# Performance work log

Measured on AMD Instinct MI355X. Metric: run time of the kernel, lower is better.

## Reference

```python
import jax, jax.numpy as jnp
import numpy as np

D_MODEL = 1024
N_HEADS = 16
D_HEAD = D_MODEL // N_HEADS


def setup_inputs() -> dict:
    key = jax.random.key(0)
    ks = jax.random.split(key, 9)
    s = 1.0 / np.sqrt(D_MODEL)
    def lin(kw, kb):
        W = jax.random.uniform(kw, (D_MODEL, D_MODEL), jnp.float32, -s, s)
        b = jax.random.uniform(kb, (D_MODEL,), jnp.float32, -s, s)
        return W, b
    Wq, bq = lin(ks[0], ks[1])
    Wk, bk = lin(ks[2], ks[3])
    Wv, bv = lin(ks[4], ks[5])
    Wo, bo = lin(ks[6], ks[7])
    x = jax.random.normal(ks[8], (4, 2048, D_MODEL), jnp.float32)
    return {"x": x, "Wq": Wq, "bq": bq, "Wk": Wk, "bk": bk,
            "Wv": Wv, "bv": bv, "Wo": Wo, "bo": bo}


def reference(x, Wq, bq, Wk, bk, Wv, bv, Wo, bo):
    B, T, C = x.shape
    # torch Linear: y = x @ W.T + b
    Q = x @ Wq.T + bq
    K = x @ Wk.T + bk
    V = x @ Wv.T + bv
    # [B, H, T, Dh]
    Q = Q.reshape(B, T, N_HEADS, D_HEAD).transpose(0, 2, 1, 3)
    K = K.reshape(B, T, N_HEADS, D_HEAD).transpose(0, 2, 1, 3)
    V = V.reshape(B, T, N_HEADS, D_HEAD).transpose(0, 2, 1, 3)
    scale = jnp.float32(np.sqrt(D_HEAD))
    scores = jnp.einsum('bhqd,bhkd->bhqk', Q, K) / scale
    causal = jnp.tril(jnp.ones((T, T), dtype=bool))  # True where allowed
    scores = jnp.where(causal, scores, jnp.float32(-jnp.inf))
    attn = jax.nn.softmax(scores, axis=-1)
    out = jnp.einsum('bhqk,bhkd->bhqd', attn, V)
    out = out.transpose(0, 2, 1, 3).reshape(B, T, C)
    return out @ Wo.T + bo
```

## Files before the change

kernel.cpp:

```cpp
#include <hip/hip_runtime.h>
#include <hip/hip_bf16.h>


typedef float f32x4 __attribute__((ext_vector_type(4)));
typedef __bf16 bf16x8 __attribute__((ext_vector_type(8)));

#define DEVI __device__ __forceinline__

#define QSCALE 0.1803368801111204f

template<int N> struct IC { static constexpr int value = N; };

DEVI ushort f2b(float x) {
  __hip_bfloat16 h = __float2bfloat16(x);
  return __builtin_bit_cast(ushort, h);
}

DEVI unsigned int pkbf(float a, float b) {
#if __has_builtin(__builtin_amdgcn_cvt_pk_bf16_f32)
  typedef __bf16 bf16x2 __attribute__((ext_vector_type(2)));
  bf16x2 r = __builtin_amdgcn_cvt_pk_bf16_f32(a, b);
  return __builtin_bit_cast(unsigned int, r);
#else
  return (unsigned int)f2b(a) | ((unsigned int)f2b(b) << 16);
#endif
}

DEVI bf16x8 ldsFrag(const ushort* p) {
  return __builtin_bit_cast(bf16x8, *(const uint4*)p);
}

DEVI f32x4 mfma16(bf16x8 a, bf16x8 b, f32x4 c) {
  return __builtin_amdgcn_mfma_f32_16x16x32_bf16(a, b, c, 0, 0, 0);
}

DEVI void gload_lds16(const ushort* g, ushort* l) {
  __builtin_amdgcn_global_load_lds(
      (const __attribute__((address_space(1))) unsigned int*)g,
      (__attribute__((address_space(3))) unsigned int*)l, 16, 0, 0);
}

__global__ void k_cvtAll(const float4* __restrict__ x,
                         const float4* __restrict__ w0, const float4* __restrict__ w1,
                         const float4* __restrict__ w2, const float4* __restrict__ w3,
                         ushort4* __restrict__ xb, ushort4* __restrict__ wcat) {
  const int blk = blockIdx.x;
  const int i = blk * 256 + threadIdx.x;
  float4 f;
  ushort4* dst;
  int di;
  if (blk < 8192) {
    f = x[i]; dst = xb; di = i;
  } else {
    const int wi = i - 8192 * 256;
    const int sel = wi >> 18;
    const float4* src = (sel == 0) ? w0 : (sel == 1) ? w1 : (sel == 2) ? w2 : w3;
    f = src[wi & 262143]; dst = wcat; di = wi;
  }
  ushort4 o;
  o.x = f2b(f.x); o.y = f2b(f.y); o.z = f2b(f.z); o.w = f2b(f.w);
  dst[di] = o;
}

template<int MODE>
__global__ __launch_bounds__(256)
void k_gemm(const ushort* __restrict__ A, const ushort* __restrict__ W,
            const float* __restrict__ b0, const float* __restrict__ b1,
            const float* __restrict__ b2, float* __restrict__ outF,
            ushort* __restrict__ oQ, ushort* __restrict__ oK, ushort* __restrict__ oV) {
  __shared__ ushort As[128 * 64];
  __shared__ ushort Bs[128 * 64];
  const int tid = threadIdx.x;
  const int wave = tid >> 6, lane = tid & 63;
  const int col = lane & 15, quad = lane >> 4;
  const int id = blockIdx.x;
  const int s_ = id >> 3;
  const int m0 = ((id & 7) * 8 + (s_ & 7)) * 128;
  const int n0 = (s_ >> 3) * 128;
  const int wm = (wave >> 1) * 64, wn = (wave & 1) * 64;
  f32x4 acc[4][4] = {};

  const int grow = lane >> 3;
  const int gchunk = ((lane & 7) ^ grow) * 8;
  const ushort* Ag = A + (size_t)(m0 + wave * 8 + grow) * 1024 + gchunk;
  const ushort* Wg = W + (size_t)(n0 + wave * 8 + grow) * 1024 + gchunk;
  ushort* AsW = &As[wave * 512];
  ushort* BsW = &Bs[wave * 512];

  const int matId = (MODE == 0) ? (n0 >> 10) : 0;
  const int cswz = col & 7;

  auto kloop = [&](auto swc) {
    constexpr bool SW = (decltype(swc)::value != 0);
    for (int k0 = 0; k0 < 1024; k0 += 64) {
      __syncthreads();
#pragma unroll
      for (int g = 0; g < 4; ++g) {
        gload_lds16(Ag + (size_t)g * 32 * 1024 + k0, AsW + g * 2048);
        gload_lds16(Wg + (size_t)g * 32 * 1024 + k0, BsW + g * 2048);
      }
      __syncthreads();
#pragma unroll
      for (int kk = 0; kk < 2; ++kk) {
        bf16x8 af[4], bfr[4];
#pragma unroll
        for (int i = 0; i < 4; ++i)
          af[i] = ldsFrag(&As[(wm + i * 16 + col) * 64 + (((kk * 4 + quad) ^ cswz) * 8)]);
#pragma unroll
        for (int j = 0; j < 4; ++j)
          bfr[j] = ldsFrag(&Bs[(wn + j * 16 + col) * 64 + (((kk * 4 + quad) ^ cswz) * 8)]);
#pragma unroll
        for (int i = 0; i < 4; ++i)
#pragma unroll
          for (int j = 0; j < 4; ++j) {
            if constexpr (SW)
              acc[i][j] = mfma16(bfr[j], af[i], acc[i][j]);
            else
              acc[i][j] = mfma16(af[i], bfr[j], acc[i][j]);
          }
      }
    }
  };

  if (MODE == 1 || matId < 2) kloop(IC<1>{}); else kloop(IC<0>{});

  if (MODE == 1) {
#pragma unroll
    for (int j = 0; j < 4; ++j) {
      const int nb = n0 + wn + j * 16 + quad * 4;
      const float4 bb = *(const float4*)&b0[nb];
#pragma unroll
      for (int i = 0; i < 4; ++i) {
        const int m = m0 + wm + i * 16 + col;
        float4 v;
        v.x = acc[i][j][0] + bb.x;
        v.y = acc[i][j][1] + bb.y;
        v.z = acc[i][j][2] + bb.z;
        v.w = acc[i][j][3] + bb.w;
        *(float4*)&outF[(size_t)m * 1024 + nb] = v;
      }
    }
  } else if (matId < 2) {
    ushort* dst = (matId == 0) ? oQ : oK;
    const float* bias = (matId == 0) ? b0 : b1;
    const float sc = (matId == 0) ? QSCALE : 1.0f;
#pragma unroll
    for (int j = 0; j < 4; ++j) {
      const int nl = ((n0 & 1023) + wn + j * 16 + quad * 4);
      const int h = nl >> 6, dh0 = nl & 63;
      const float4 bb = *(const float4*)&bias[nl];
#pragma unroll
      for (int i = 0; i < 4; ++i) {
        const int m = m0 + wm + i * 16 + col;
        const int b = m >> 11, t = m & 2047;
        ushort4 pk;
        pk.x = f2b((acc[i][j][0] + bb.x) * sc);
        pk.y = f2b((acc[i][j][1] + bb.y) * sc);
        pk.z = f2b((acc[i][j][2] + bb.z) * sc);
        pk.w = f2b((acc[i][j][3] + bb.w) * sc);
        *(ushort4*)&dst[(((size_t)(b * 16 + h) * 2048) + t) * 64 + dh0] = pk;
      }
    }
  } else {
#pragma unroll
    for (int j = 0; j < 4; ++j) {
      const int nl = ((n0 & 1023) + wn + j * 16 + col);
      const int h = nl >> 6, dh = nl & 63;
      const float bn = b2[nl];
#pragma unroll
      for (int i = 0; i < 4; ++i) {
        const int mBase = m0 + wm + i * 16 + quad * 4;
        const int b = mBase >> 11, t = mBase & 2047;
        ushort4 pk;
        pk.x = f2b(acc[i][j][0] + bn);
        pk.y = f2b(acc[i][j][1] + bn);
        pk.z = f2b(acc[i][j][2] + bn);
        pk.w = f2b(acc[i][j][3] + bn);
        *(ushort4*)&oV[(((size_t)(b * 16 + h) * 64) + dh) * 2048 + t] = pk;
      }
    }
  }
}

__global__ __launch_bounds__(512, 1)
void k_attn(const ushort* __restrict__ Q, const ushort* __restrict__ K,
            const ushort* __restrict__ Vt, ushort* __restrict__ AO) {
  __shared__ ushort Ks[2 * 4096];
  __shared__ ushort Vs[2 * 4096];
  __shared__ ushort Os[512];
  __shared__ ushort Ps[16 * 16 * 72];
  const int tid = threadIdx.x;
  const int wave = tid >> 6, lane = tid & 63;
  const int col = lane & 15, quad = lane >> 4;
  const int id = blockIdx.x;
  const int bh = (id & 7) * 8 + ((id >> 3) & 7);
  const int pr = id >> 6;
  const ushort* Qg = Q + (size_t)bh * 2048 * 64;
  const ushort* Kg = K + (size_t)bh * 2048 * 64;
  const ushort* Vg = Vt + (size_t)bh * 64 * 2048;

  if (tid < 128) {
    const ushort one = 0x3F80;
    ushort4 zv;
    if (tid < 8) { zv.x = one; zv.y = one; zv.z = one; zv.w = one; }
    else         { zv.x = 0;   zv.y = 0;   zv.z = 0;   zv.w = 0;   }
    *(ushort4*)&Os[tid * 4] = zv;
  }

  const int grow = lane >> 3;
  const int gchunk = ((lane & 7) ^ grow) * 8;
  const int cswz = col & 7;
  ushort* Pw0 = &Ps[((wave * 2 + 0) * 16 + col) * 72];
  ushort* Pw1 = &Ps[((wave * 2 + 1) * 16 + col) * 72];

  for (int pp = 0; pp < 2; ++pp) {
    const int t = pp ? (7 - pr) : pr;
    const int q0 = t * 256;

    bf16x8 qf[2][2];
#pragma unroll
    for (int s = 0; s < 2; ++s) {
      const ushort* p = Qg + (q0 + wave * 32 + s * 16 + col) * 64 + quad * 8;
      qf[s][0] = __builtin_bit_cast(bf16x8, *(const uint4*)p);
      qf[s][1] = __builtin_bit_cast(bf16x8, *(const uint4*)(p + 32));
    }

    f32x4 o[2][4] = {};
    f32x4 la[2] = {};

    const ushort* kPtr = Kg + (wave * 8 + grow) * 64 + gchunk;
    const ushort* vPtr = Vg + (size_t)(wave * 8 + grow) * 2048 + gchunk;

    auto stage = [&](auto bufc) {
      constexpr int BUF = decltype(bufc)::value;
      gload_lds16(kPtr, &Ks[BUF * 4096 + wave * 512]);
      gload_lds16(vPtr, &Vs[BUF * 4096 + wave * 512]);
      kPtr += 64 * 64;
      vPtr += 64;
    };

    auto step = [&](auto bufc, auto maskc, int j0) {
      constexpr int BUF = decltype(bufc)::value;
      constexpr bool MASKED = (decltype(maskc)::value != 0);
      const ushort* Kb = &Ks[BUF * 4096];
      const ushort* Vb = &Vs[BUF * 4096];
      bf16x8 kf[4][2];
#pragma unroll
      for (int i = 0; i < 4; ++i) {
        kf[i][0] = ldsFrag(&Kb[(i * 16 + col) * 64 + (((0 * 4 + quad) ^ cswz) * 8)]);
        kf[i][1] = ldsFrag(&Kb[(i * 16 + col) * 64 + (((1 * 4 + quad) ^ cswz) * 8)]);
      }
#pragma unroll
      for (int s = 0; s < 2; ++s) {
        ushort* Pw = s ? Pw1 : Pw0;
        const int dlim = MASKED ? (q0 + wave * 32 + s * 16 + col - j0 - quad * 4) : 0;
#pragma unroll
        for (int i = 0; i < 4; ++i) {
          f32x4 z = {0.f, 0.f, 0.f, 0.f};
          f32x4 sv = mfma16(kf[i][0], qf[s][0], z);
          sv = mfma16(kf[i][1], qf[s][1], sv);
          if (MASKED) {
#pragma unroll
            for (int r = 0; r < 4; ++r)
              if (i * 16 + r > dlim) sv[r] = -1e30f;
          }
          f32x4 pv;
#pragma unroll
          for (int r = 0; r < 4; ++r) pv[r] = __builtin_amdgcn_exp2f(sv[r]);
          uint2 pk;
          pk.x = pkbf(pv[0], pv[1]);
          pk.y = pkbf(pv[2], pv[3]);
          *(uint2*)&Pw[i * 16 + quad * 4] = pk;
        }
      }
      bf16x8 osf = ldsFrag(&Os[col * 32 + quad * 8]);
#pragma unroll
      for (int c = 0; c < 2; ++c) {
        bf16x8 pb0 = ldsFrag(&Pw0[c * 32 + quad * 8]);
        bf16x8 pb1 = ldsFrag(&Pw1[c * 32 + quad * 8]);
        la[0] = mfma16(osf, pb0, la[0]);
        la[1] = mfma16(osf, pb1, la[1]);
#pragma unroll
        for (int i = 0; i < 4; ++i) {
          bf16x8 vf = ldsFrag(&Vb[(i * 16 + col) * 64 + (((c * 4 + quad) ^ cswz) * 8)]);
          o[0][i] = mfma16(vf, pb0, o[0][i]);
          o[1][i] = mfma16(vf, pb1, o[1][i]);
        }
      }
    };

    __syncthreads();
    stage(IC<0>{});
    for (int it2 = 0; it2 < 2 * t; ++it2) {
      __syncthreads();
      stage(IC<1>{});
      step(IC<0>{}, IC<0>{}, 0);
      __syncthreads();
      stage(IC<0>{});
      step(IC<1>{}, IC<0>{}, 0);
    }
    __syncthreads();
    stage(IC<1>{});
    step(IC<0>{}, IC<1>{}, q0);
    __syncthreads();
    stage(IC<0>{});
    if (wave >= 2) step(IC<1>{}, IC<1>{}, q0 + 64);
    __syncthreads();
    stage(IC<1>{});
    if (wave >= 4) step(IC<0>{}, IC<1>{}, q0 + 128);
    __syncthreads();
    if (wave >= 6) step(IC<1>{}, IC<1>{}, q0 + 192);

    const float invs[2] = {1.0f / __shfl(la[0][0], col), 1.0f / __shfl(la[1][0], col)};
    const int b = bh >> 4, h = bh & 15;
#pragma unroll
    for (int s = 0; s < 2; ++s) {
      const float inv = invs[s];
      const int tq = q0 + wave * 32 + s * 16 + col;
      ushort* dst = AO + (size_t)(b * 2048 + tq) * 1024 + h * 64;
#pragma unroll
      for (int i = 0; i < 4; ++i) {
        f32x4 v = o[s][i];
        ushort4 pk;
        pk.x = f2b(v[0] * inv);
        pk.y = f2b(v[1] * inv);
        pk.z = f2b(v[2] * inv);
        pk.w = f2b(v[3] * inv);
        *(ushort4*)&dst[i * 16 + quad * 4] = pk;
      }
    }
  }
}

extern "C" void kernel_launch(void* const* d_in, const int* in_sizes, int n_in,
                              void* d_out, int out_size, void* d_ws, size_t ws_size,
                              hipStream_t stream) {
  const float* x  = (const float*)d_in[0];
  const float* Wq = (const float*)d_in[1];
  const float* bq = (const float*)d_in[2];
  const float* Wk = (const float*)d_in[3];
  const float* bk = (const float*)d_in[4];
  const float* Wv = (const float*)d_in[5];
  const float* bv = (const float*)d_in[6];
  const float* Wo = (const float*)d_in[7];
  const float* bo = (const float*)d_in[8];
  float* out = (float*)d_out;

  char* ws = (char*)d_ws;
  ushort* xb    = (ushort*)ws;
  ushort* Wcat  = (ushort*)(ws + (size_t)16 * 1024 * 1024);
  ushort* Wob   = Wcat + (size_t)3 * 1024 * 1024;
  ushort* Qh    = (ushort*)(ws + (size_t)24 * 1024 * 1024);
  ushort* Kh    = Qh + (size_t)8192 * 1024;
  ushort* Vt    = Kh + (size_t)8192 * 1024;
  ushort* AO    = Vt + (size_t)8192 * 1024;

  k_cvtAll<<<12288, 256, 0, stream>>>((const float4*)x,
                                      (const float4*)Wq, (const float4*)Wk,
                                      (const float4*)Wv, (const float4*)Wo,
                                      (ushort4*)xb, (ushort4*)Wcat);

  k_gemm<0><<<1536, 256, 0, stream>>>(xb, Wcat, bq, bk, bv, nullptr, Qh, Kh, Vt);

  k_attn<<<256, 512, 0, stream>>>(Qh, Kh, Vt, AO);

  k_gemm<1><<<512, 256, 0, stream>>>(AO, Wob, bo, nullptr, nullptr, out,
                                     nullptr, nullptr, nullptr);
}
```

Before: 247.6 us.

## Enlarge GEMM tiles with triple-buffered pipeline and split attention into more blocks

The GEMM kernels move to 256x256 tiles with 512 threads, a K-step of 32, and a three-stage LDS buffer ring. Global loads are interleaved with MFMA work using sched barriers, priority hints and explicit vmcnt waits, so memory latency overlaps compute and operands are reused more per tile. The attention kernel now gives each block one query tile instead of two paired ones, launching twice as many blocks with higher occupancy bounds to balance the causal workload. Larger tiles reduce the number of blocks (384 and 128), which risks leaving CUs idle on a large GPU and raises register pressure.

```diff
diff --git a/kernel.cpp b/kernel.cpp
--- a/kernel.cpp
+++ b/kernel.cpp
@@ -39,6 +39,10 @@
       (const __attribute__((address_space(1))) unsigned int*)g,
       (__attribute__((address_space(3))) unsigned int*)l, 16, 0, 0);
 }
+
+#define SBAR() do { __builtin_amdgcn_sched_barrier(0); \
+                    __builtin_amdgcn_s_barrier();      \
+                    __builtin_amdgcn_sched_barrier(0); } while (0)
 
 __global__ void k_cvtAll(const float4* __restrict__ x,
                          const float4* __restrict__ w0, const float4* __restrict__ w1,
@@ -63,52 +67,66 @@
 }
 
 template<int MODE>
-__global__ __launch_bounds__(256)
+__global__ __launch_bounds__(512, 2)
 void k_gemm(const ushort* __restrict__ A, const ushort* __restrict__ W,
             const float* __restrict__ b0, const float* __restrict__ b1,
             const float* __restrict__ b2, float* __restrict__ outF,
             ushort* __restrict__ oQ, ushort* __restrict__ oK, ushort* __restrict__ oV) {
-  __shared__ ushort As[128 * 64];
-  __shared__ ushort Bs[128 * 64];
+  __shared__ ushort As[3][256 * 32];
+  __shared__ ushort Bs[3][256 * 32];
   const int tid = threadIdx.x;
   const int wave = tid >> 6, lane = tid & 63;
   const int col = lane & 15, quad = lane >> 4;
+  constexpr int NTI = (MODE == 0) ? 12 : 4;
+  constexpr int PER = NTI * 4;
   const int id = blockIdx.x;
-  const int s_ = id >> 3;
-  const int m0 = ((id & 7) * 8 + (s_ & 7)) * 128;
-  const int n0 = (s_ >> 3) * 128;
-  const int wm = (wave >> 1) * 64, wn = (wave & 1) * 64;
-  f32x4 acc[4][4] = {};
-
-  const int grow = lane >> 3;
-  const int gchunk = ((lane & 7) ^ grow) * 8;
-  const ushort* Ag = A + (size_t)(m0 + wave * 8 + grow) * 1024 + gchunk;
-  const ushort* Wg = W + (size_t)(n0 + wave * 8 + grow) * 1024 + gchunk;
-  ushort* AsW = &As[wave * 512];
-  ushort* BsW = &Bs[wave * 512];
+  const int L = (id & 7) * PER + (id >> 3);
+  const int m0 = (L & 31) * 256;
+  const int n0 = (L >> 5) * 256;
+  const int wm = (wave >> 2) * 128, wn = (wave & 3) * 64;
+
+  const int riu = lane >> 2;
+  const int gch = ((lane & 3) ^ ((lane >> 3) & 3)) * 8;
+  const ushort* Ag = A + (size_t)(m0 + wave * 32 + riu) * 1024 + gch;
+  const ushort* Wg = W + (size_t)(n0 + wave * 32 + riu) * 1024 + gch;
 
   const int matId = (MODE == 0) ? (n0 >> 10) : 0;
-  const int cswz = col & 7;
+  const int ko = (quad ^ ((col >> 1) & 3)) * 8;
+
+  f32x4 acc[8][4] = {};
+  bf16x8 bfr[4];
+
+  auto stageA = [&](int t2, int buf) {
+    const int ks = t2 * 32;
+    gload_lds16(Ag + ks,             &As[buf][(wave * 32) * 32]);
+    gload_lds16(Ag + 16 * 1024 + ks, &As[buf][(wave * 32 + 16) * 32]);
+  };
+  auto stageB = [&](int t2, int buf) {
+    const int ks = t2 * 32;
+    gload_lds16(Wg + ks,             &Bs[buf][(wave * 32) * 32]);
+    gload_lds16(Wg + 16 * 1024 + ks, &Bs[buf][(wave * 32 + 16) * 32]);
+  };
 
   auto kloop = [&](auto swc) {
     constexpr bool SW = (decltype(swc)::value != 0);
-    for (int k0 = 0; k0 < 1024; k0 += 64) {
-      __syncthreads();
-#pragma unroll
-      for (int g = 0; g < 4; ++g) {
-        gload_lds16(Ag + (size_t)g * 32 * 1024 + k0, AsW + g * 2048);
-        gload_lds16(Wg + (size_t)g * 32 * 1024 + k0, BsW + g * 2048);
-      }
-      __syncthreads();
-#pragma unroll
-      for (int kk = 0; kk < 2; ++kk) {
-        bf16x8 af[4], bfr[4];
+    stageA(0, 0); stageB(0, 0);
+    stageA(1, 1); stageB(1, 1);
+    asm volatile("s_waitcnt vmcnt(4)" ::: "memory");
+    SBAR();
+    int r0 = 0, r1 = 1, r2 = 2;
+    for (int t = 0; t < 32; ++t) {
+      const bool st = (t < 30);
+      {
+        bf16x8 af[4];
 #pragma unroll
         for (int i = 0; i < 4; ++i)
-          af[i] = ldsFrag(&As[(wm + i * 16 + col) * 64 + (((kk * 4 + quad) ^ cswz) * 8)]);
+          af[i] = ldsFrag(&As[r0][(wm + i * 16 + col) * 32 + ko]);
 #pragma unroll
         for (int j = 0; j < 4; ++j)
-          bfr[j] = ldsFrag(&Bs[(wn + j * 16 + col) * 64 + (((kk * 4 + quad) ^ cswz) * 8)]);
+          bfr[j] = ldsFrag(&Bs[r0][(wn + j * 16 + col) * 32 + ko]);
+        if (st) stageA(t + 2, r2);
+        SBAR();
+        __builtin_amdgcn_s_setprio(1);
 #pragma unroll
         for (int i = 0; i < 4; ++i)
 #pragma unroll
@@ -118,7 +136,32 @@
             else
               acc[i][j] = mfma16(af[i], bfr[j], acc[i][j]);
           }
-      }
+        __builtin_amdgcn_s_setprio(0);
+        SBAR();
+      }
+      {
+        bf16x8 af[4];
+#pragma unroll
+        for (int i = 0; i < 4; ++i)
+          af[i] = ldsFrag(&As[r0][(wm + 64 + i * 16 + col) * 32 + ko]);
+        if (st) stageB(t + 2, r2);
+        SBAR();
+        __builtin_amdgcn_s_setprio(1);
+#pragma unroll
+        for (int i = 0; i < 4; ++i)
+#pragma unroll
+          for (int j = 0; j < 4; ++j) {
+            if constexpr (SW)
+              acc[4 + i][j] = mfma16(bfr[j], af[i], acc[4 + i][j]);
+            else
+              acc[4 + i][j] = mfma16(af[i], bfr[j], acc[4 + i][j]);
+          }
+        __builtin_amdgcn_s_setprio(0);
+        if (t < 30)       { asm volatile("s_waitcnt vmcnt(4)" ::: "memory"); }
+        else if (t == 30) { asm volatile("s_waitcnt vmcnt(0)" ::: "memory"); }
+        SBAR();
+      }
+      const int tmp = r0; r0 = r1; r1 = r2; r2 = tmp;
     }
   };
 
@@ -126,63 +169,69 @@
 
   if (MODE == 1) {
 #pragma unroll
-    for (int j = 0; j < 4; ++j) {
-      const int nb = n0 + wn + j * 16 + quad * 4;
-      const float4 bb = *(const float4*)&b0[nb];
-#pragma unroll
-      for (int i = 0; i < 4; ++i) {
-        const int m = m0 + wm + i * 16 + col;
-        float4 v;
-        v.x = acc[i][j][0] + bb.x;
-        v.y = acc[i][j][1] + bb.y;
-        v.z = acc[i][j][2] + bb.z;
-        v.w = acc[i][j][3] + bb.w;
-        *(float4*)&outF[(size_t)m * 1024 + nb] = v;
-      }
-    }
+    for (int h = 0; h < 2; ++h)
+#pragma unroll
+      for (int j = 0; j < 4; ++j) {
+        const int nb = n0 + wn + j * 16 + quad * 4;
+        const float4 bb = *(const float4*)&b0[nb];
+#pragma unroll
+        for (int i = 0; i < 4; ++i) {
+          const int m = m0 + wm + h * 64 + i * 16 + col;
+          float4 v;
+          v.x = acc[h * 4 + i][j][0] + bb.x;
+          v.y = acc[h * 4 + i][j][1] + bb.y;
+          v.z = acc[h * 4 + i][j][2] + bb.z;
+          v.w = acc[h * 4 + i][j][3] + bb.w;
+          *(float4*)&outF[(size_t)m * 1024 + nb] = v;
+        }
+      }
   } else if (matId < 2) {
     ushort* dst = (matId == 0) ? oQ : oK;
     const float* bias = (matId == 0) ? b0 : b1;
     const float sc = (matId == 0) ? QSCALE : 1.0f;
 #pragma unroll
-    for (int j = 0; j < 4; ++j) {
-      const int nl = ((n0 & 1023) + wn + j * 16 + quad * 4);
-      const int h = nl >> 6, dh0 = nl & 63;
-      const float4 bb = *(const float4*)&bias[nl];
-#pragma unroll
-      for (int i = 0; i < 4; ++i) {
-        const int m = m0 + wm + i * 16 + col;
-        const int b = m >> 11, t = m & 2047;
-        ushort4 pk;
-        pk.x = f2b((acc[i][j][0] + bb.x) * sc);
-        pk.y = f2b((acc[i][j][1] + bb.y) * sc);
-        pk.z = f2b((acc[i][j][2] + bb.z) * sc);
-        pk.w = f2b((acc[i][j][3] + bb.w) * sc);
-        *(ushort4*)&dst[(((size_t)(b * 16 + h) * 2048) + t) * 64 + dh0] = pk;
-      }
-    }
+    for (int h = 0; h < 2; ++h)
+#pragma unroll
+      for (int j = 0; j < 4; ++j) {
+        const int nl = (n0 & 1023) + wn + j * 16 + quad * 4;
+        const int hh = nl >> 6, dh0 = nl & 63;
+        const float4 bb = *(const float4*)&bias[nl];
+#pragma unroll
+        for (int i = 0; i < 4; ++i) {
+          const int m = m0 + wm + h * 64 + i * 16 + col;
+          const int b = m >> 11, t = m & 2047;
+          ushort4 pk;
+          pk.x = f2b((acc[h * 4 + i][j][0] + bb.x) * sc);
+          pk.y = f2b((acc[h * 4 + i][j][1] + bb.y) * sc);
+          pk.z = f2b((acc[h * 4 + i][j][2] + bb.z) * sc);
+          pk.w = f2b((acc[h * 4 + i][j][3] + bb.w) * sc);
+          *(ushort4*)&dst[(((size_t)(b * 16 + hh) * 2048) + t) * 64 + dh0] = pk;
+        }
+      }
   } else {
 #pragma unroll
-    for (int j = 0; j < 4; ++j) {
-      const int nl = ((n0 & 1023) + wn + j * 16 + col);
-      const int h = nl >> 6, dh = nl & 63;
-      const float bn = b2[nl];
-#pragma unroll
-      for (int i = 0; i < 4; ++i) {
-        const int mBase = m0 + wm + i * 16 + quad * 4;
-        const int b = mBase >> 11, t = mBase & 2047;
-        ushort4 pk;
-        pk.x = f2b(acc[i][j][0] + bn);
-        pk.y = f2b(acc[i][j][1] + bn);
-        pk.z = f2b(acc[i][j][2] + bn);
-        pk.w = f2b(acc[i][j][3] + bn);
-        *(ushort4*)&oV[(((size_t)(b * 16 + h) * 64) + dh) * 2048 + t] = pk;
-      }
-    }
-  }
-}
-
-__global__ __launch_bounds__(512, 1)
+    for (int h = 0; h < 2; ++h)
+#pragma unroll
+      for (int j = 0; j < 4; ++j) {
+        const int nl = (n0 & 1023) + wn + j * 16 + col;
+        const int hh = nl >> 6, dh = nl & 63;
+        const float bn = b2[nl];
+#pragma unroll
+        for (int i = 0; i < 4; ++i) {
+          const int mBase = m0 + wm + h * 64 + i * 16 + quad * 4;
+          const int b = mBase >> 11, t = mBase & 2047;
+          ushort4 pk;
+          pk.x = f2b(acc[h * 4 + i][j][0] + bn);
+          pk.y = f2b(acc[h * 4 + i][j][1] + bn);
+          pk.z = f2b(acc[h * 4 + i][j][2] + bn);
+          pk.w = f2b(acc[h * 4 + i][j][3] + bn);
+          *(ushort4*)&oV[(((size_t)(b * 16 + hh) * 64) + dh) * 2048 + t] = pk;
+        }
+      }
+  }
+}
+
+__global__ __launch_bounds__(512, 4)
 void k_attn(const ushort* __restrict__ Q, const ushort* __restrict__ K,
             const ushort* __restrict__ Vt, ushort* __restrict__ AO) {
   __shared__ ushort Ks[2 * 4096];
@@ -194,7 +243,9 @@
   const int col = lane & 15, quad = lane >> 4;
   const int id = blockIdx.x;
   const int bh = (id & 7) * 8 + ((id >> 3) & 7);
-  const int pr = id >> 6;
+  const int g = id >> 6;
+  const int t = (id < 256) ? (7 - g) : (g - 4);
+  const int q0 = t * 256;
   const ushort* Qg = Q + (size_t)bh * 2048 * 64;
   const ushort* Kg = K + (size_t)bh * 2048 * 64;
   const ushort* Vg = Vt + (size_t)bh * 64 * 2048;
@@ -213,121 +264,116 @@
   ushort* Pw0 = &Ps[((wave * 2 + 0) * 16 + col) * 72];
   ushort* Pw1 = &Ps[((wave * 2 + 1) * 16 + col) * 72];
 
-  for (int pp = 0; pp < 2; ++pp) {
-    const int t = pp ? (7 - pr) : pr;
-    const int q0 = t * 256;
-
-    bf16x8 qf[2][2];
+  bf16x8 qf[2][2];
+#pragma unroll
+  for (int s = 0; s < 2; ++s) {
+    const ushort* p = Qg + (q0 + wave * 32 + s * 16 + col) * 64 + quad * 8;
+    qf[s][0] = __builtin_bit_cast(bf16x8, *(const uint4*)p);
+    qf[s][1] = __builtin_bit_cast(bf16x8, *(const uint4*)(p + 32));
+  }
+
+  f32x4 o[2][4] = {};
+  f32x4 la[2] = {};
+
+  const ushort* kPtr = Kg + (wave * 8 + grow) * 64 + gchunk;
+  const ushort* vPtr = Vg + (size_t)(wave * 8 + grow) * 2048 + gchunk;
+
+  auto stage = [&](auto bufc) {
+    constexpr int BUF = decltype(bufc)::value;
+    gload_lds16(kPtr, &Ks[BUF * 4096 + wave * 512]);
+    gload_lds16(vPtr, &Vs[BUF * 4096 + wave * 512]);
+    kPtr += 64 * 64;
+    vPtr += 64;
+  };
+
+  auto step = [&](auto bufc, auto maskc, int j0) {
+    constexpr int BUF = decltype(bufc)::value;
+    constexpr bool MASKED = (decltype(maskc)::value != 0);
+    const ushort* Kb = &Ks[BUF * 4096];
+    const ushort* Vb = &Vs[BUF * 4096];
+    bf16x8 kf[4][2];
+#pragma unroll
+    for (int i = 0; i < 4; ++i) {
+      kf[i][0] = ldsFrag(&Kb[(i * 16 + col) * 64 + (((0 * 4 + quad) ^ cswz) * 8)]);
+      kf[i][1] = ldsFrag(&Kb[(i * 16 + col) * 64 + (((1 * 4 + quad) ^ cswz) * 8)]);
+    }
 #pragma unroll
     for (int s = 0; s < 2; ++s) {
-      const ushort* p = Qg + (q0 + wave * 32 + s * 16 + col) * 64 + quad * 8;
-      qf[s][0] = __builtin_bit_cast(bf16x8, *(const uint4*)p);
-      qf[s][1] = __builtin_bit_cast(bf16x8, *(const uint4*)(p + 32));
+      ushort* Pw = s ? Pw1 : Pw0;
+      const int dlim = MASKED ? (q0 + wave * 32 + s * 16 + col - j0 - quad * 4) : 0;
+#pragma unroll
+      for (int i = 0; i < 4; ++i) {
+        f32x4 z = {0.f, 0.f, 0.f, 0.f};
+        f32x4 sv = mfma16(kf[i][0], qf[s][0], z);
+        sv = mfma16(kf[i][1], qf[s][1], sv);
+        if (MASKED) {
+#pragma unroll
+          for (int r = 0; r < 4; ++r)
+            if (i * 16 + r > dlim) sv[r] = -1e30f;
+        }
+        f32x4 pv;
+#pragma unroll
+        for (int r = 0; r < 4; ++r) pv[r] = __builtin_amdgcn_exp2f(sv[r]);
+        uint2 pk;
+        pk.x = pkbf(pv[0], pv[1]);
+        pk.y = pkbf(pv[2], pv[3]);
+        *(uint2*)&Pw[i * 16 + quad * 4] = pk;
+      }
     }
-
-    f32x4 o[2][4] = {};
-    f32x4 la[2] = {};
-
-    const ushort* kPtr = Kg + (wave * 8 + grow) * 64 + gchunk;
-    const ushort* vPtr = Vg + (size_t)(wave * 8 + grow) * 2048 + gchunk;
-
-    auto stage = [&](auto bufc) {
-      constexpr int BUF = decltype(bufc)::value;
-      gload_lds16(kPtr, &Ks[BUF * 4096 + wave * 512]);
-      gload_lds16(vPtr, &Vs[BUF * 4096 + wave * 512]);
-      kPtr += 64 * 64;
-      vPtr += 64;
-    };
-
-    auto step = [&](auto bufc, auto maskc, int j0) {
-      constexpr int BUF = decltype(bufc)::value;
-      constexpr bool MASKED = (decltype(maskc)::value != 0);
-      const ushort* Kb = &Ks[BUF * 4096];
-      const ushort* Vb = &Vs[BUF * 4096];
-      bf16x8 kf[4][2];
+    bf16x8 osf = ldsFrag(&Os[col * 32 + quad * 8]);
+#pragma unroll
+    for (int c = 0; c < 2; ++c) {
+      bf16x8 pb0 = ldsFrag(&Pw0[c * 32 + quad * 8]);
+      bf16x8 pb1 = ldsFrag(&Pw1[c * 32 + quad * 8]);
+      la[0] = mfma16(osf, pb0, la[0]);
+      la[1] = mfma16(osf, pb1, la[1]);
 #pragma unroll
       for (int i = 0; i < 4; ++i) {
-        kf[i][0] = ldsFrag(&Kb[(i * 16 + col) * 64 + (((0 * 4 + quad) ^ cswz) * 8)]);
-        kf[i][1] = ldsFrag(&Kb[(i * 16 + col) * 64 + (((1 * 4 + quad) ^ cswz) * 8)]);
-      }
-#pragma unroll
-      for (int s = 0; s < 2; ++s) {
-        ushort* Pw = s ? Pw1 : Pw0;
-        const int dlim = MASKED ? (q0 + wave * 32 + s * 16 + col - j0 - quad * 4) : 0;
-#pragma unroll
-        for (int i = 0; i < 4; ++i) {
-          f32x4 z = {0.f, 0.f, 0.f, 0.f};
-          f32x4 sv = mfma16(kf[i][0], qf[s][0], z);
-          sv = mfma16(kf[i][1], qf[s][1], sv);
-          if (MASKED) {
-#pragma unroll
-            for (int r = 0; r < 4; ++r)
-              if (i * 16 + r > dlim) sv[r] = -1e30f;
-          }
-          f32x4 pv;
-#pragma unroll
-          for (int r = 0; r < 4; ++r) pv[r] = __builtin_amdgcn_exp2f(sv[r]);
-          uint2 pk;
-          pk.x = pkbf(pv[0], pv[1]);
-          pk.y = pkbf(pv[2], pv[3]);
-          *(uint2*)&Pw[i * 16 + quad * 4] = pk;
-        }
-      }
-      bf16x8 osf = ldsFrag(&Os[col * 32 + quad * 8]);
-#pragma unroll
-      for (int c = 0; c < 2; ++c) {
-        bf16x8 pb0 = ldsFrag(&Pw0[c * 32 + quad * 8]);
-        bf16x8 pb1 = ldsFrag(&Pw1[c * 32 + quad * 8]);
-        la[0] = mfma16(osf, pb0, la[0]);
-        la[1] = mfma16(osf, pb1, la[1]);
-#pragma unroll
-        for (int i = 0; i < 4; ++i) {
-          bf16x8 vf = ldsFrag(&Vb[(i * 16 + col) * 64 + (((c * 4 + quad) ^ cswz) * 8)]);
-          o[0][i] = mfma16(vf, pb0, o[0][i]);
-          o[1][i] = mfma16(vf, pb1, o[1][i]);
-        }
-      }
-    };
-
+        bf16x8 vf = ldsFrag(&Vb[(i * 16 + col) * 64 + (((c * 4 + quad) ^ cswz) * 8)]);
+        o[0][i] = mfma16(vf, pb0, o[0][i]);
+        o[1][i] = mfma16(vf, pb1, o[1][i]);
+      }
+    }
+  };
+
+  __syncthreads();
+  stage(IC<0>{});
+  for (int it2 = 0; it2 < 2 * t; ++it2) {
+    __syncthreads();
+    stage(IC<1>{});
+    step(IC<0>{}, IC<0>{}, 0);
     __syncthreads();
     stage(IC<0>{});
-    for (int it2 = 0; it2 < 2 * t; ++it2) {
-      __syncthreads();
-      stage(IC<1>{});
-      step(IC<0>{}, IC<0>{}, 0);
-      __syncthreads();
-      stage(IC<0>{});
-      step(IC<1>{}, IC<0>{}, 0);
-    }
-    __syncthreads();
-    stage(IC<1>{});
-    step(IC<0>{}, IC<1>{}, q0);
-    __syncthreads();
-    stage(IC<0>{});
-    if (wave >= 2) step(IC<1>{}, IC<1>{}, q0 + 64);
-    __syncthreads();
-    stage(IC<1>{});
-    if (wave >= 4) step(IC<0>{}, IC<1>{}, q0 + 128);
-    __syncthreads();
-    if (wave >= 6) step(IC<1>{}, IC<1>{}, q0 + 192);
-
-    const float invs[2] = {1.0f / __shfl(la[0][0], col), 1.0f / __shfl(la[1][0], col)};
-    const int b = bh >> 4, h = bh & 15;
-#pragma unroll
-    for (int s = 0; s < 2; ++s) {
-      const float inv = invs[s];
-      const int tq = q0 + wave * 32 + s * 16 + col;
-      ushort* dst = AO + (size_t)(b * 2048 + tq) * 1024 + h * 64;
-#pragma unroll
-      for (int i = 0; i < 4; ++i) {
-        f32x4 v = o[s][i];
-        ushort4 pk;
-        pk.x = f2b(v[0] * inv);
-        pk.y = f2b(v[1] * inv);
-        pk.z = f2b(v[2] * inv);
-        pk.w = f2b(v[3] * inv);
-        *(ushort4*)&dst[i * 16 + quad * 4] = pk;
-      }
+    step(IC<1>{}, IC<0>{}, 0);
+  }
+  __syncthreads();
+  stage(IC<1>{});
+  step(IC<0>{}, IC<1>{}, q0);
+  __syncthreads();
+  stage(IC<0>{});
+  if (wave >= 2) step(IC<1>{}, IC<1>{}, q0 + 64);
+  __syncthreads();
+  stage(IC<1>{});
+  if (wave >= 4) step(IC<0>{}, IC<1>{}, q0 + 128);
+  __syncthreads();
+  if (wave >= 6) step(IC<1>{}, IC<1>{}, q0 + 192);
+
+  const float invs[2] = {1.0f / __shfl(la[0][0], col), 1.0f / __shfl(la[1][0], col)};
+  const int b = bh >> 4, h = bh & 15;
+#pragma unroll
+  for (int s = 0; s < 2; ++s) {
+    const float inv = invs[s];
+    const int tq = q0 + wave * 32 + s * 16 + col;
+    ushort* dst = AO + (size_t)(b * 2048 + tq) * 1024 + h * 64;
+#pragma unroll
+    for (int i = 0; i < 4; ++i) {
+      f32x4 v = o[s][i];
+      ushort4 pk;
+      pk.x = f2b(v[0] * inv);
+      pk.y = f2b(v[1] * inv);
+      pk.z = f2b(v[2] * inv);
+      pk.w = f2b(v[3] * inv);
+      *(ushort4*)&dst[i * 16 + quad * 4] = pk;
     }
   }
 }
@@ -360,10 +406,10 @@
                                       (const float4*)Wv, (const float4*)Wo,
                                       (ushort4*)xb, (ushort4*)Wcat);
 
-  k_gemm<0><<<1536, 256, 0, stream>>>(xb, Wcat, bq, bk, bv, nullptr, Qh, Kh, Vt);
-
-  k_attn<<<256, 512, 0, stream>>>(Qh, Kh, Vt, AO);
-
-  k_gemm<1><<<512, 256, 0, stream>>>(AO, Wob, bo, nullptr, nullptr, out,
+  k_gemm<0><<<384, 512, 0, stream>>>(xb, Wcat, bq, bk, bv, nullptr, Qh, Kh, Vt);
+
+  k_attn<<<512, 512, 0, stream>>>(Qh, Kh, Vt, AO);
+
+  k_gemm<1><<<128, 512, 0, stream>>>(AO, Wob, bo, nullptr, nullptr, out,
                                      nullptr, nullptr, nullptr);
 }
```

Result: slower. 276.4 us (+11.6%).
